# Kernel optimization log

Measured on AMD Instinct MI355X. Metric: run time of the kernel, lower is better.

Reference implementation:

```python
import jax, jax.numpy as jnp
import numpy as np

B, T, D, H = 2, 2048, 1024, 16
HD = D // H

def setup_inputs() -> dict:
    key = jax.random.key(0)
    ks = jax.random.split(key, 5)
    fan = D
    bound_w = float(np.sqrt(6.0 / fan))  # kaiming_uniform-ish scale
    return {
        "x": jax.random.normal(ks[0], (B, T, D), dtype=jnp.float32),
        "W_qkv": jax.random.uniform(ks[1], (3 * D, D), minval=-bound_w, maxval=bound_w, dtype=jnp.float32),
        "b_qkv": jax.random.uniform(ks[2], (3 * D,), minval=-bound_w, maxval=bound_w, dtype=jnp.float32),
        "W_proj": jax.random.uniform(ks[3], (D, D), minval=-bound_w, maxval=bound_w, dtype=jnp.float32),
        "b_proj": jax.random.uniform(ks[4], (D,), minval=-bound_w, maxval=bound_w, dtype=jnp.float32),
    }

def reference(x, W_qkv, b_qkv, W_proj, b_proj):
    Bx, Tx, C = x.shape
    h, hd = H, C // H
    qkv = x @ W_qkv.T + b_qkv                      # (B,T,3C)
    q, k, v = jnp.split(qkv, 3, axis=-1)
    # (B,T,C) -> (B,h,T,hd)
    q = q.reshape(Bx, Tx, h, hd).transpose(0, 2, 1, 3)
    k = k.reshape(Bx, Tx, h, hd).transpose(0, 2, 1, 3)
    v = v.reshape(Bx, Tx, h, hd).transpose(0, 2, 1, 3)
    scale = hd ** -0.5
    scores = jnp.einsum('bhqd,bhkd->bhqk', q, k) * scale
    causal = jnp.tril(jnp.ones((Tx, Tx), dtype=bool))
    scores = jnp.where(causal, scores, -jnp.inf)
    weights = jax.nn.softmax(scores, axis=-1)      # stable softmax, same math
    out = jnp.einsum('bhqk,bhkd->bhqd', weights, v)
    out = out.transpose(0, 2, 1, 3).reshape(Bx, Tx, C)
    return out @ W_proj.T + b_proj
```

## Files before the change

kernel.cpp:

```cpp
#include <hip/hip_runtime.h>

typedef unsigned short u16;
typedef __attribute__((ext_vector_type(8))) short bf16x8;
typedef __attribute__((ext_vector_type(4))) float f32x4;

#define Bb 2
#define Tt 2048
#define Dd 1024
#define Hh 16
#define HD 64
#define NTOK (Bb*Tt)
#define QKVN (3*Dd)

__device__ __forceinline__ u16 f2b(float f) {
    unsigned u = __float_as_uint(f);
    unsigned r = (u + 0x7fffu + ((u >> 16) & 1u)) >> 16;
    return (u16)r;
}

__device__ __forceinline__ void g2l16(const u16* g, u16* l) {
    __builtin_amdgcn_global_load_lds(
        (const __attribute__((address_space(1))) unsigned int*)g,
        (__attribute__((address_space(3))) unsigned int*)l,
        16, 0, 0);
}

__device__ __forceinline__ unsigned pk2(float lo, float hi) {
    return __builtin_amdgcn_perm(__float_as_uint(hi), __float_as_uint(lo), 0x07060302u);
}

#define N4X  (NTOK * Dd / 4)
#define N4WQ (3 * Dd * Dd / 4)
#define N4WP (Dd * Dd / 4)
__global__ void cvt_all(const float* __restrict__ x, const float* __restrict__ wq,
                        const float* __restrict__ wp, u16* __restrict__ xb,
                        u16* __restrict__ wqb, u16* __restrict__ wpb) {
    int i = blockIdx.x * blockDim.x + threadIdx.x;
    const float* src; u16* dst; int j;
    if (i < N4X)                { src = x;  dst = xb;  j = i; }
    else if (i < N4X + N4WQ)    { src = wq; dst = wqb; j = i - N4X; }
    else                        { src = wp; dst = wpb; j = i - N4X - N4WQ; }
    float4 f = ((const float4*)src)[j];
    ushort4 o;
    o.x = f2b(f.x); o.y = f2b(f.y); o.z = f2b(f.z); o.w = f2b(f.w);
    ((ushort4*)dst)[j] = o;
}

template<int MODE>
__global__ __launch_bounds__(256, 2)
void gemm_bt(const u16* __restrict__ A, const u16* __restrict__ Bt,
             const float* __restrict__ bias, int M, int N, int K,
             u16* __restrict__ C16, float* __restrict__ Co) {
    __shared__ alignas(16) u16 As[128 * 32];
    __shared__ alignas(16) u16 Bs[128 * 32];
    const int tid = threadIdx.x;
    const int wave = tid >> 6, lane = tid & 63;
    const int quad = lane >> 4, l16 = lane & 15;
    const int wm = (wave & 1) * 64, wn = (wave >> 1) * 64;
    const int m0 = blockIdx.x * 128, n0 = blockIdx.y * 128;
    const int lrow = lane >> 2, lcol = (lane & 3) << 3;

    f32x4 acc[4][4];
#pragma unroll
    for (int i = 0; i < 4; ++i)
#pragma unroll
        for (int j = 0; j < 4; ++j)
            acc[i][j] = (f32x4){0.f, 0.f, 0.f, 0.f};

    for (int k0 = 0; k0 < K; k0 += 32) {
#pragma unroll
        for (int c = 0; c < 2; ++c) {
            const int rb = (c * 4 + wave) * 16;
            g2l16(A  + (size_t)(m0 + rb + lrow) * K + k0 + lcol, &As[rb * 32 + (lane << 3)]);
            g2l16(Bt + (size_t)(n0 + rb + lrow) * K + k0 + lcol, &Bs[rb * 32 + (lane << 3)]);
        }
        __syncthreads();
        bf16x8 a[4], b[4];
#pragma unroll
        for (int i = 0; i < 4; ++i)
            a[i] = *(const bf16x8*)(&As[(wm + i * 16 + l16) * 32 + quad * 8]);
#pragma unroll
        for (int i = 0; i < 4; ++i)
            b[i] = *(const bf16x8*)(&Bs[(wn + i * 16 + l16) * 32 + quad * 8]);
#pragma unroll
        for (int i = 0; i < 4; ++i)
#pragma unroll
            for (int j = 0; j < 4; ++j)
                acc[i][j] = __builtin_amdgcn_mfma_f32_16x16x32_bf16(a[i], b[j], acc[i][j], 0, 0, 0);
        __syncthreads();
    }

    float b4[4];
#pragma unroll
    for (int j = 0; j < 4; ++j) b4[j] = bias[n0 + wn + j * 16 + l16];

#pragma unroll
    for (int i = 0; i < 4; ++i) {
#pragma unroll
        for (int j = 0; j < 4; ++j) {
#pragma unroll
            for (int r = 0; r < 4; ++r) {
                int m = m0 + wm + i * 16 + quad * 4 + r;
                int n = n0 + wn + j * 16 + l16;
                float v = acc[i][j][r] + b4[j];
                if (MODE == 0) C16[(size_t)m * N + n] = f2b(v);
                else           Co[(size_t)m * N + n] = v;
            }
        }
    }
}

__global__ __launch_bounds__(256)
void transpose_v(const u16* __restrict__ qkv, u16* __restrict__ Vt) {
    __shared__ u16 Ls[64 * 66];
    const int t0 = blockIdx.x * 64, bh = blockIdx.y;
    const int hh = bh & (Hh - 1), bidx = bh >> 4;
    const int tid = threadIdx.x;
    const int r = tid >> 2, c = (tid & 3) << 4;
    const u16* src = qkv + (size_t)(bidx * Tt + t0 + r) * QKVN + 2 * Dd + hh * HD + c;
    *(uint4*)(&Ls[r * 66 + c]) = *(const uint4*)src;
    *(uint4*)(&Ls[r * 66 + c + 8]) = *(const uint4*)(src + 8);
    __syncthreads();
    const int d = tid >> 2, tc = (tid & 3) << 4;
    u16 tmp[16];
#pragma unroll
    for (int j = 0; j < 16; ++j) tmp[j] = Ls[(tc + j) * 66 + d];
    u16* dst = Vt + ((size_t)bh * HD + d) * Tt + t0 + tc;
    *(uint4*)(dst)     = *(const uint4*)(tmp);
    *(uint4*)(dst + 8) = *(const uint4*)(tmp + 8);
}

#define LKP 80
#define PSP 84
#define FMX 24.0f

__global__ __launch_bounds__(256, 4)
void attn_fwd(const u16* __restrict__ qkv, const u16* __restrict__ Vt,
              u16* __restrict__ Ao) {
    const int qt = 31 - (int)blockIdx.x;
    const int bh = blockIdx.y;
    const int hh = bh & (Hh - 1), bidx = bh >> 4;
    const u16* Qp = qkv + (size_t)bidx * Tt * QKVN + hh * HD;
    const u16* Kp = Qp + Dd;
    const u16* Vp = Vt + (size_t)bh * HD * Tt;
    const int tid = threadIdx.x;
    const int wave = tid >> 6, lane = tid & 63;
    const int quad = lane >> 4, l16 = lane & 15;

    __shared__ alignas(16) u16 Ks[64 * LKP];
    __shared__ alignas(16) u16 Vs[64 * LKP];
    __shared__ alignas(16) u16 Ps[4][16 * PSP];
    u16* Pw = &Ps[wave][0];

    const int srow = tid >> 3, scol = (tid & 7) << 3;
    const float sc = 0.125f * 1.44269504f;

    const int q0 = qt * 64;
    const int qrow_g = q0 + wave * 16 + l16;
    bf16x8 aq[2];
#pragma unroll
    for (int kk = 0; kk < 2; ++kk)
        aq[kk] = *(const bf16x8*)(Qp + (size_t)qrow_g * QKVN + kk * 32 + quad * 8);

    f32x4 o[4];
#pragma unroll
    for (int nt = 0; nt < 4; ++nt) o[nt] = (f32x4){0.f, 0.f, 0.f, 0.f};
    float lsum = 0.f;
    const int nit = qt + 1;

    uint4 kreg0, kreg1, vreg0, vreg1;
    kreg0 = *(const uint4*)(Kp + (size_t)srow * QKVN + scol);
    kreg1 = *(const uint4*)(Kp + (size_t)(srow + 32) * QKVN + scol);
    vreg0 = *(const uint4*)(Vp + (size_t)srow * Tt + scol);
    vreg1 = *(const uint4*)(Vp + (size_t)(srow + 32) * Tt + scol);

    for (int kt = 0; kt < nit; ++kt) {
        const int k0 = kt * 64;
        *(uint4*)(&Ks[srow * LKP + scol]) = kreg0;
        *(uint4*)(&Ks[(srow + 32) * LKP + scol]) = kreg1;
        *(uint4*)(&Vs[srow * LKP + scol]) = vreg0;
        *(uint4*)(&Vs[(srow + 32) * LKP + scol]) = vreg1;
        __syncthreads();
        if (kt + 1 < nit) {
            const int kn = k0 + 64;
            kreg0 = *(const uint4*)(Kp + (size_t)(kn + srow) * QKVN + scol);
            kreg1 = *(const uint4*)(Kp + (size_t)(kn + srow + 32) * QKVN + scol);
            vreg0 = *(const uint4*)(Vp + (size_t)srow * Tt + kn + scol);
            vreg1 = *(const uint4*)(Vp + (size_t)(srow + 32) * Tt + kn + scol);
        }

        f32x4 s[4];
#pragma unroll
        for (int nt = 0; nt < 4; ++nt) {
            f32x4 z = (f32x4){0.f, 0.f, 0.f, 0.f};
#pragma unroll
            for (int kk = 0; kk < 2; ++kk) {
                bf16x8 ak = *(const bf16x8*)(&Ks[(nt * 16 + l16) * LKP + kk * 32 + quad * 8]);
                z = __builtin_amdgcn_mfma_f32_16x16x32_bf16(ak, aq[kk], z, 0, 0, 0);
            }
            s[nt] = z;
        }

        if (kt == qt) {
#pragma unroll
            for (int nt = 0; nt < 4; ++nt)
#pragma unroll
                for (int r = 0; r < 4; ++r) {
                    int key = k0 + nt * 16 + quad * 4 + r;
                    float t = __builtin_fmaf(s[nt][r], sc, -FMX);
                    t = (key <= qrow_g) ? t : -200.0f;
                    float p = exp2f(t);
                    s[nt][r] = p;
                    lsum += p;
                }
        } else {
#pragma unroll
            for (int nt = 0; nt < 4; ++nt)
#pragma unroll
                for (int r = 0; r < 4; ++r) {
                    float p = exp2f(__builtin_fmaf(s[nt][r], sc, -FMX));
                    s[nt][r] = p;
                    lsum += p;
                }
        }

#pragma unroll
        for (int nt = 0; nt < 4; ++nt) {
            uint2 d;
            d.x = pk2(s[nt][0], s[nt][1]);
            d.y = pk2(s[nt][2], s[nt][3]);
            *(uint2*)(&Pw[l16 * PSP + nt * 16 + quad * 4]) = d;
        }

#pragma unroll
        for (int kk = 0; kk < 2; ++kk) {
            bf16x8 bp = *(const bf16x8*)(&Pw[l16 * PSP + kk * 32 + quad * 8]);
#pragma unroll
            for (int nt = 0; nt < 4; ++nt) {
                bf16x8 av = *(const bf16x8*)(&Vs[(nt * 16 + l16) * LKP + kk * 32 + quad * 8]);
                o[nt] = __builtin_amdgcn_mfma_f32_16x16x32_bf16(av, bp, o[nt], 0, 0, 0);
            }
        }
        __syncthreads();
    }

    lsum += __shfl_xor(lsum, 16, 64);
    lsum += __shfl_xor(lsum, 32, 64);
    const float rinv = 1.0f / lsum;
    u16* orow = Ao + ((size_t)bidx * Tt + qrow_g) * Dd + hh * HD;
#pragma unroll
    for (int nt = 0; nt < 4; ++nt) {
        ushort4 p4;
        p4.x = f2b(o[nt][0] * rinv); p4.y = f2b(o[nt][1] * rinv);
        p4.z = f2b(o[nt][2] * rinv); p4.w = f2b(o[nt][3] * rinv);
        *(ushort4*)(orow + nt * 16 + quad * 4) = p4;
    }
}

extern "C" void kernel_launch(void* const* d_in, const int* in_sizes, int n_in,
                              void* d_out, int out_size, void* d_ws, size_t ws_size,
                              hipStream_t stream) {
    const float* x      = (const float*)d_in[0];
    const float* W_qkv  = (const float*)d_in[1];
    const float* b_qkv  = (const float*)d_in[2];
    const float* W_proj = (const float*)d_in[3];
    const float* b_proj = (const float*)d_in[4];
    float* out = (float*)d_out;

    char* ws = (char*)d_ws;
    u16* Wprojb = (u16*)(ws);
    u16* Wqkvb  = (u16*)(ws + (2u << 20));
    u16* xb     = (u16*)(ws + (8u << 20));
    u16* qkvb   = (u16*)(ws + (16u << 20));
    u16* Vtb    = (u16*)(ws + (40u << 20));
    u16* attnb  = (u16*)(ws + (2u << 20));

    cvt_all<<<(N4X + N4WQ + N4WP) / 256, 256, 0, stream>>>(x, W_qkv, W_proj, xb, Wqkvb, Wprojb);

    {
        dim3 grid(NTOK / 128, QKVN / 128);
        gemm_bt<0><<<grid, 256, 0, stream>>>(xb, Wqkvb, b_qkv, NTOK, QKVN, Dd,
                                             qkvb, nullptr);
    }
    {
        dim3 grid(Tt / 64, Bb * Hh);
        transpose_v<<<grid, 256, 0, stream>>>(qkvb, Vtb);
    }
    {
        dim3 grid(32, Bb * Hh);
        attn_fwd<<<grid, 256, 0, stream>>>(qkvb, Vtb, attnb);
    }
    {
        dim3 grid(NTOK / 128, Dd / 128);
        gemm_bt<1><<<grid, 256, 0, stream>>>(attnb, Wprojb, b_proj, NTOK, Dd, Dd,
                                             nullptr, out);
    }
}
```

Measured before the change: 216.1 us.

## Split long causal attention rows into KV chunks with a merge kernel

```diff
diff --git a/kernel.cpp b/kernel.cpp
--- a/kernel.cpp
+++ b/kernel.cpp
@@ -16,6 +16,13 @@
     unsigned u = __float_as_uint(f);
     unsigned r = (u + 0x7fffu + ((u >> 16) & 1u)) >> 16;
     return (u16)r;
+}
+__device__ __forceinline__ u16 f2h(float f) {
+    _Float16 h = (_Float16)f;
+    return __builtin_bit_cast(u16, h);
+}
+__device__ __forceinline__ float h2f(u16 v) {
+    return (float)__builtin_bit_cast(_Float16, v);
 }
 
 __device__ __forceinline__ void g2l16(const u16* g, u16* l) {
@@ -133,12 +140,20 @@
 #define LKP 80
 #define PSP 84
 #define FMX 24.0f
-
-__global__ __launch_bounds__(256, 4)
+#define NCH 48
+
+__global__ __launch_bounds__(256, 5)
 void attn_fwd(const u16* __restrict__ qkv, const u16* __restrict__ Vt,
-              u16* __restrict__ Ao) {
-    const int qt = 31 - (int)blockIdx.x;
-    const int bh = blockIdx.y;
+              u16* __restrict__ Opart, float* __restrict__ lsumP) {
+    const int ci = blockIdx.x, bh = blockIdx.y;
+    int qt, c0;
+    if (ci < 16)      { qt = 31 - ci;        c0 = 0; }
+    else if (ci < 32) { qt = 31 - (ci - 16); c0 = 1; }
+    else              { qt = 15 - (ci - 32); c0 = 0; }
+    const int kt_lo = c0 * 16;
+    const int nit_full = qt + 1;
+    const int kt_hi = nit_full < kt_lo + 16 ? nit_full : kt_lo + 16;
+
     const int hh = bh & (Hh - 1), bidx = bh >> 4;
     const u16* Qp = qkv + (size_t)bidx * Tt * QKVN + hh * HD;
     const u16* Kp = Qp + Dd;
@@ -166,22 +181,24 @@
 #pragma unroll
     for (int nt = 0; nt < 4; ++nt) o[nt] = (f32x4){0.f, 0.f, 0.f, 0.f};
     float lsum = 0.f;
-    const int nit = qt + 1;
 
     uint4 kreg0, kreg1, vreg0, vreg1;
-    kreg0 = *(const uint4*)(Kp + (size_t)srow * QKVN + scol);
-    kreg1 = *(const uint4*)(Kp + (size_t)(srow + 32) * QKVN + scol);
-    vreg0 = *(const uint4*)(Vp + (size_t)srow * Tt + scol);
-    vreg1 = *(const uint4*)(Vp + (size_t)(srow + 32) * Tt + scol);
-
-    for (int kt = 0; kt < nit; ++kt) {
+    {
+        const int kb = kt_lo * 64;
+        kreg0 = *(const uint4*)(Kp + (size_t)(kb + srow) * QKVN + scol);
+        kreg1 = *(const uint4*)(Kp + (size_t)(kb + srow + 32) * QKVN + scol);
+        vreg0 = *(const uint4*)(Vp + (size_t)srow * Tt + kb + scol);
+        vreg1 = *(const uint4*)(Vp + (size_t)(srow + 32) * Tt + kb + scol);
+    }
+
+    for (int kt = kt_lo; kt < kt_hi; ++kt) {
         const int k0 = kt * 64;
         *(uint4*)(&Ks[srow * LKP + scol]) = kreg0;
         *(uint4*)(&Ks[(srow + 32) * LKP + scol]) = kreg1;
         *(uint4*)(&Vs[srow * LKP + scol]) = vreg0;
         *(uint4*)(&Vs[(srow + 32) * LKP + scol]) = vreg1;
         __syncthreads();
-        if (kt + 1 < nit) {
+        if (kt + 1 < kt_hi) {
             const int kn = k0 + 64;
             kreg0 = *(const uint4*)(Kp + (size_t)(kn + srow) * QKVN + scol);
             kreg1 = *(const uint4*)(Kp + (size_t)(kn + srow + 32) * QKVN + scol);
@@ -247,14 +264,60 @@
     lsum += __shfl_xor(lsum, 16, 64);
     lsum += __shfl_xor(lsum, 32, 64);
     const float rinv = 1.0f / lsum;
-    u16* orow = Ao + ((size_t)bidx * Tt + qrow_g) * Dd + hh * HD;
+    const size_t slot = (size_t)bh * NCH + ci;
+    if (quad == 0)
+        lsumP[slot * 64 + wave * 16 + l16] = lsum;
+    u16* oslot = Opart + slot * 4096 + (wave * 16 + l16) * 64;
 #pragma unroll
     for (int nt = 0; nt < 4; ++nt) {
         ushort4 p4;
-        p4.x = f2b(o[nt][0] * rinv); p4.y = f2b(o[nt][1] * rinv);
-        p4.z = f2b(o[nt][2] * rinv); p4.w = f2b(o[nt][3] * rinv);
-        *(ushort4*)(orow + nt * 16 + quad * 4) = p4;
-    }
+        p4.x = f2h(o[nt][0] * rinv); p4.y = f2h(o[nt][1] * rinv);
+        p4.z = f2h(o[nt][2] * rinv); p4.w = f2h(o[nt][3] * rinv);
+        *(ushort4*)(oslot + nt * 16 + quad * 4) = p4;
+    }
+}
+
+__global__ __launch_bounds__(256)
+void attn_finalize(const u16* __restrict__ Opart, const float* __restrict__ lsumP,
+                   u16* __restrict__ Ao) {
+    const int qt = blockIdx.x, bh = blockIdx.y;
+    const int hh = bh & (Hh - 1), bidx = bh >> 4;
+    const int tid = threadIdx.x;
+    const int qrow = tid >> 2, off = (tid & 3) << 4;
+    int s0, s1;
+    if (qt >= 16) { s0 = 31 - qt; s1 = 16 + (31 - qt); }
+    else          { s0 = 32 + (15 - qt); s1 = -1; }
+
+    const size_t slot0 = (size_t)bh * NCH + s0;
+    float l0 = lsumP[slot0 * 64 + qrow];
+    u16 buf[16];
+    {
+        const u16* p = Opart + slot0 * 4096 + qrow * 64 + off;
+        *(uint4*)(buf) = *(const uint4*)(p);
+        *(uint4*)(buf + 8) = *(const uint4*)(p + 8);
+    }
+    float acc[16];
+#pragma unroll
+    for (int j = 0; j < 16; ++j) acc[j] = h2f(buf[j]) * l0;
+    float l = l0;
+    if (s1 >= 0) {
+        const size_t slot1 = (size_t)bh * NCH + s1;
+        float l1 = lsumP[slot1 * 64 + qrow];
+        l += l1;
+        const u16* p = Opart + slot1 * 4096 + qrow * 64 + off;
+        u16 b2[16];
+        *(uint4*)(b2) = *(const uint4*)(p);
+        *(uint4*)(b2 + 8) = *(const uint4*)(p + 8);
+#pragma unroll
+        for (int j = 0; j < 16; ++j) acc[j] = __builtin_fmaf(h2f(b2[j]), l1, acc[j]);
+    }
+    const float rinv = 1.0f / l;
+    u16 ob[16];
+#pragma unroll
+    for (int j = 0; j < 16; ++j) ob[j] = f2b(acc[j] * rinv);
+    u16* dst = Ao + ((size_t)bidx * Tt + qt * 64 + qrow) * Dd + hh * HD + off;
+    *(uint4*)(dst) = *(const uint4*)(ob);
+    *(uint4*)(dst + 8) = *(const uint4*)(ob + 8);
 }
 
 extern "C" void kernel_launch(void* const* d_in, const int* in_sizes, int n_in,
@@ -268,12 +331,14 @@
     float* out = (float*)d_out;
 
     char* ws = (char*)d_ws;
-    u16* Wprojb = (u16*)(ws);
-    u16* Wqkvb  = (u16*)(ws + (2u << 20));
-    u16* xb     = (u16*)(ws + (8u << 20));
-    u16* qkvb   = (u16*)(ws + (16u << 20));
-    u16* Vtb    = (u16*)(ws + (40u << 20));
-    u16* attnb  = (u16*)(ws + (2u << 20));
+    u16*   Wprojb = (u16*)(ws);
+    u16*   Wqkvb  = (u16*)(ws + (2u << 20));
+    u16*   xb     = (u16*)(ws + (8u << 20));
+    u16*   Opart  = (u16*)(ws + (2u << 20));
+    float* lsumP  = (float*)(ws + (14u << 20));
+    u16*   qkvb   = (u16*)(ws + (16u << 20));
+    u16*   attnb  = (u16*)(ws + (16u << 20));
+    u16*   Vtb    = (u16*)(ws + (40u << 20));
 
     cvt_all<<<(N4X + N4WQ + N4WP) / 256, 256, 0, stream>>>(x, W_qkv, W_proj, xb, Wqkvb, Wprojb);
 
@@ -287,8 +352,12 @@
         transpose_v<<<grid, 256, 0, stream>>>(qkvb, Vtb);
     }
     {
+        dim3 grid(NCH, Bb * Hh);
+        attn_fwd<<<grid, 256, 0, stream>>>(qkvb, Vtb, Opart, lsumP);
+    }
+    {
         dim3 grid(32, Bb * Hh);
-        attn_fwd<<<grid, 256, 0, stream>>>(qkvb, Vtb, attnb);
+        attn_finalize<<<grid, 256, 0, stream>>>(Opart, lsumP, attnb);
     }
     {
         dim3 grid(NTOK / 128, Dd / 128);
```

Result: faster. 207.0 us (-4.2%).
